# Performance work log

Measured on AMD Instinct MI355X. Metric: run time of the kernel, lower is better.

## Reference

```python
import jax, jax.numpy as jnp
import numpy as np

N = 100000
E = 1600000
F_IN = 64
HID = 64
OUT = 64


def _sage_conv(x, src, dst, w_l, b_l, w_r):
    # PyG SAGEConv (mean aggr): out = lin_l(mean_{j in N(i)} x_j) + lin_r(x_i)
    msgs = x[src]                                             # [E, F] gather
    summed = jax.ops.segment_sum(msgs, dst, num_segments=N)   # [N, F]
    ones = jnp.ones((src.shape[0],), dtype=x.dtype)
    cnt = jax.ops.segment_sum(ones, dst, num_segments=N)      # [N]
    mean = summed / jnp.maximum(cnt, 1.0)[:, None]
    return mean @ w_l + b_l + x @ w_r


def setup_inputs() -> dict:
    key = jax.random.key(0)
    ks = jax.random.split(key, 12)
    sc = lambda f: 1.0 / np.sqrt(f)
    inp = {
        "h": jax.random.normal(ks[0], (N, F_IN), dtype=jnp.float32),
        "edge_index": jax.random.randint(ks[1], (2, E), 0, N, dtype=jnp.int64),
        # conv1: lin_l (with bias) and lin_r (no bias), weights stored [in, out]
        "w1_l": jax.random.normal(ks[2], (F_IN, HID), dtype=jnp.float32) * sc(F_IN),
        "b1_l": jnp.zeros((HID,), dtype=jnp.float32),
        "w1_r": jax.random.normal(ks[3], (F_IN, HID), dtype=jnp.float32) * sc(F_IN),
        "w_lin1": jax.random.normal(ks[4], (HID, HID), dtype=jnp.float32) * sc(HID),
        "b_lin1": jnp.zeros((HID,), dtype=jnp.float32),
        "w2_l": jax.random.normal(ks[5], (HID, HID), dtype=jnp.float32) * sc(HID),
        "b2_l": jnp.zeros((HID,), dtype=jnp.float32),
        "w2_r": jax.random.normal(ks[6], (HID, HID), dtype=jnp.float32) * sc(HID),
        "w_lin2": jax.random.normal(ks[7], (HID, OUT), dtype=jnp.float32) * sc(HID),
        "b_lin2": jnp.zeros((OUT,), dtype=jnp.float32),
    }
    return inp


def reference(h, edge_index, w1_l, b1_l, w1_r, w_lin1, b_lin1,
              w2_l, b2_l, w2_r, w_lin2, b_lin2):
    src, dst = edge_index[0], edge_index[1]
    x = jax.nn.relu(_sage_conv(h, src, dst, w1_l, b1_l, w1_r))
    x = jax.nn.relu(x @ w_lin1 + b_lin1)
    x = jax.nn.relu(_sage_conv(x, src, dst, w2_l, b2_l, w2_r))
    x = x @ w_lin2 + b_lin2
    return x
```

## Files before the change

### kernel.cpp

```cpp
#include <hip/hip_runtime.h>
#include <hip/hip_fp16.h>

#define FEAT   64
#define BSHIFT 8
#define BNODES 256
#define MAXB   512
#define CHUNK  4096
#define REGION 5120
#define ECAP   2048

typedef _Float16 half8 __attribute__((ext_vector_type(8)));
typedef float  float4v __attribute__((ext_vector_type(4)));

__global__ __launch_bounds__(256) void setup_kernel(
    const float* __restrict__ h, __half* __restrict__ h16, int n4, int CB,
    const float* w0, const float* w1, const float* w2,
    const float* w3, const float* w4, const float* w5,
    __half* __restrict__ wT, int* __restrict__ bcur)
{
    int b = blockIdx.x;
    if (b < CB) {
        int i = b * 256 + threadIdx.x;
        if (i < n4) {
            float4 v = ((const float4*)h)[i];
            union { uint2 u; __half2 h2[2]; } r;
            r.h2[0] = __floats2half2_rn(v.x, v.y);
            r.h2[1] = __floats2half2_rn(v.z, v.w);
            ((uint2*)h16)[i] = r.u;
        }
    } else if (b < CB + 96) {
        int bb = b - CB;
        int m = bb >> 4;
        int idx = ((bb & 15) << 8) | threadIdx.x;
        const float* src = m==0?w0 : m==1?w1 : m==2?w2 : m==3?w3 : m==4?w4 : w5;
        int o = idx >> 6, i = idx & 63;
        wT[m * 4096 + o * 64 + i] = __float2half(src[i * 64 + o]);
    } else {
        bcur[threadIdx.x] = 0;
        bcur[threadIdx.x + 256] = 0;
    }
}

__global__ __launch_bounds__(512) void partition_kernel(
    const int* __restrict__ src, const int* __restrict__ dst,
    int* __restrict__ bcur, int* __restrict__ pedge, int E)
{
    __shared__ int cnt[MAXB];
    __shared__ int sa[MAXB], sb[MAXB];
    __shared__ int gb[MAXB];
    __shared__ int lcur[MAXB];
    __shared__ int stage[CHUNK];
    __shared__ int tgt[CHUNK];

    int tid = threadIdx.x;
    cnt[tid] = 0;
    __syncthreads();

    int base = blockIdx.x * CHUNK;
    int vals[8];
    int bs[8];
#pragma unroll
    for (int i = 0; i < 8; i++) {
        int e = base + tid + i * 512;
        bs[i] = -1;
        if (e < E) {
            int s_ = src[e];
            int d_ = dst[e];
            int b  = d_ >> BSHIFT;
            bs[i]  = b;
            vals[i] = s_ | ((d_ & (BNODES - 1)) << 20);
            atomicAdd(&cnt[b], 1);
        }
    }
    __syncthreads();

    sa[tid] = cnt[tid];
    __syncthreads();
    int* cur = sa; int* nxt = sb;
    for (int off = 1; off < MAXB; off <<= 1) {
        nxt[tid] = cur[tid] + ((tid >= off) ? cur[tid - off] : 0);
        __syncthreads();
        int* tmp = cur; cur = nxt; nxt = tmp;
    }
    {
        int c = cnt[tid];
        int lo = cur[tid] - c;
        int gbase = c ? atomicAdd(&bcur[tid], c) : 0;
        if (gbase > REGION) gbase = REGION;
        gb[tid]   = tid * REGION + gbase - lo;
        lcur[tid] = lo;
    }
    __syncthreads();

#pragma unroll
    for (int i = 0; i < 8; i++) {
        if (bs[i] >= 0) {
            int pos = atomicAdd(&lcur[bs[i]], 1);
            stage[pos] = vals[i];
            tgt[pos]   = gb[bs[i]];
        }
    }
    __syncthreads();

    int cn = min(CHUNK, E - base);
    for (int i = tid; i < cn; i += 512)
        pedge[tgt[i] + i] = stage[i];
}

__global__ __launch_bounds__(512) void buildcsr_kernel(
    const int* __restrict__ pedge, const int* __restrict__ bcur,
    unsigned* __restrict__ rowinfo, int* __restrict__ csr, int N)
{
    __shared__ int stg[REGION];
    __shared__ int srt[REGION];
    __shared__ int hist[BNODES], scn[BNODES], lcur[BNODES];
    int b = blockIdx.x;
    int tid = threadIdx.x;
    int beg = b * REGION;
    int cnt = min(bcur[b], REGION);

    if (tid < BNODES) hist[tid] = 0;
    __syncthreads();

    for (int i = tid; i < cnt; i += 512) {
        int p = pedge[beg + i];
        stg[i] = p;
        atomicAdd(&hist[p >> 20], 1);
    }
    __syncthreads();

    int v = 0;
    if (tid < BNODES) { v = hist[tid]; scn[tid] = v; }
    __syncthreads();
    for (int off = 1; off < BNODES; off <<= 1) {
        int t = 0;
        if (tid < BNODES && tid >= off) t = scn[tid - off];
        __syncthreads();
        if (tid < BNODES) scn[tid] += t;
        __syncthreads();
    }
    if (tid < BNODES) {
        int excl = scn[tid] - v;
        int node = (b << BSHIFT) + tid;
        if (node < N)
            rowinfo[node] = (unsigned)(beg + excl) | ((unsigned)v << 21);
        lcur[tid] = excl;
    }
    __syncthreads();

    for (int i = tid; i < cnt; i += 512) {
        int p = stg[i];
        int pos = atomicAdd(&lcur[p >> 20], 1);
        srt[pos] = p & 0xFFFFF;
    }
    __syncthreads();
    for (int i = tid; i < cnt; i += 512)
        csr[beg + i] = srt[i];
}

__global__ __launch_bounds__(256, 4) void fused_layer_kernel(
    const __half* __restrict__ x, const unsigned* __restrict__ rowinfo,
    const int* __restrict__ csr_src,
    const __half* __restrict__ wlT, const __half* __restrict__ wrT,
    const __half* __restrict__ w2T,
    const float* __restrict__ b1, const float* __restrict__ b2,
    float* __restrict__ out_f, __half* __restrict__ out_h,
    int n, int relu_out)
{
    __shared__ __attribute__((aligned(16))) _Float16 sbuf[64][72];
    __shared__ int sedge[ECAP];

    int tid  = threadIdx.x;
    int wave = tid >> 6;
    int lane = tid & 63;
    int sg   = tid >> 4;
    int gg   = (tid >> 3) & 1;
    int s8   = tid & 7;
    int r    = lane & 15;
    int q    = lane >> 4;
    int base = blockIdx.x * 64 + wave * 16;
    int node0 = blockIdx.x * 64;

    int arow = min(base + r, n - 1);
    const half8* xrow = (const half8*)(x + (size_t)arow * FEAT);
    half8 Ax0 = xrow[q], Ax1 = xrow[4 + q];

    unsigned i0 = rowinfo[node0];
    unsigned iL = rowinfo[min(node0 + 63, n - 1)];
    int beg0 = (int)(i0 & 0x1FFFFFu);
    int span = (int)(iL & 0x1FFFFFu) + (int)(iL >> 21) - beg0;

    unsigned infos[4];
#pragma unroll
    for (int i = 0; i < 4; i++) {
        int node = node0 + sg * 4 + i;
        infos[i] = (node < n) ? rowinfo[node] : 0u;
    }

    int spanc = min(span, ECAP);
    for (int i = tid; i < spanc; i += 256)
        sedge[i] = csr_src[beg0 + i];
    __syncthreads();

    int lbeg[4], deg4[4];
    int itmax = 0;
#pragma unroll
    for (int i = 0; i < 4; i++) {
        deg4[i] = (int)(infos[i] >> 21);
        lbeg[i] = deg4[i] ? (int)(infos[i] & 0x1FFFFFu) - beg0 : 0;
        itmax = max(itmax, (deg4[i] + 3) >> 2);
    }
    float acc[4][8];
#pragma unroll
    for (int i = 0; i < 4; i++)
#pragma unroll
        for (int t = 0; t < 8; t++) acc[i][t] = 0.f;

    for (int it = 0; it < itmax; ++it) {
        uint4  rr[8];
        float  ww[8];
#pragma unroll
        for (int i = 0; i < 4; i++) {
            int o0 = (it << 2) + gg;
            int o1 = o0 + 2;
            bool v0 = o0 < deg4[i];
            bool v1 = o1 < deg4[i];
            int l0 = lbeg[i] + (v0 ? o0 : 0);
            int l1 = lbeg[i] + (v1 ? o1 : 0);
            int j0 = v0 ? ((l0 < ECAP) ? sedge[l0] : csr_src[beg0 + l0]) : 0;
            int j1 = v1 ? ((l1 < ECAP) ? sedge[l1] : csr_src[beg0 + l1]) : 0;
            rr[2*i]   = ((const uint4*)(x + (size_t)j0 * FEAT))[s8];
            rr[2*i+1] = ((const uint4*)(x + (size_t)j1 * FEAT))[s8];
            ww[2*i]   = v0 ? 1.0f : 0.0f;
            ww[2*i+1] = v1 ? 1.0f : 0.0f;
        }
#pragma unroll
        for (int k = 0; k < 8; k++) {
            union { uint4 u; __half2 h2[4]; } rv; rv.u = rr[k];
            int a = k >> 1;
#pragma unroll
            for (int t = 0; t < 4; t++) {
                float2 f = __half22float2(rv.h2[t]);
                acc[a][2*t]   = fmaf(ww[k], f.x, acc[a][2*t]);
                acc[a][2*t+1] = fmaf(ww[k], f.y, acc[a][2*t+1]);
            }
        }
    }

#pragma unroll
    for (int i = 0; i < 4; i++) {
#pragma unroll
        for (int t = 0; t < 8; t++)
            acc[i][t] += __shfl_xor(acc[i][t], 8, 64);
        if (gg == 0) {
            int deg = deg4[i];
            float inv = deg ? 1.0f / (float)deg : 0.0f;
            union { uint4 u; __half2 h2[4]; } o;
            o.h2[0] = __floats2half2_rn(acc[i][0]*inv, acc[i][1]*inv);
            o.h2[1] = __floats2half2_rn(acc[i][2]*inv, acc[i][3]*inv);
            o.h2[2] = __floats2half2_rn(acc[i][4]*inv, acc[i][5]*inv);
            o.h2[3] = __floats2half2_rn(acc[i][6]*inv, acc[i][7]*inv);
            int ln = sg * 4 + i;
            *(uint4*)&sbuf[ln][s8 * 8] = o.u;
        }
    }
    __syncthreads();

    union { uint4 u4; half8 h; } Am0u, Am1u;
    Am0u.u4 = *(const uint4*)&sbuf[wave * 16 + r][q * 8];
    Am1u.u4 = *(const uint4*)&sbuf[wave * 16 + r][(4 + q) * 8];

    float4v acc1[4];
#pragma unroll
    for (int c = 0; c < 4; c++) {
        float bv = b1[c * 16 + r];
        acc1[c] = (float4v){bv, bv, bv, bv};
        const half8* bl = (const half8*)(wlT + (size_t)(c * 16 + r) * FEAT);
        const half8* br = (const half8*)(wrT + (size_t)(c * 16 + r) * FEAT);
        acc1[c] = __builtin_amdgcn_mfma_f32_16x16x32_f16(Am0u.h, bl[q],     acc1[c], 0, 0, 0);
        acc1[c] = __builtin_amdgcn_mfma_f32_16x16x32_f16(Am1u.h, bl[4 + q], acc1[c], 0, 0, 0);
        acc1[c] = __builtin_amdgcn_mfma_f32_16x16x32_f16(Ax0,    br[q],     acc1[c], 0, 0, 0);
        acc1[c] = __builtin_amdgcn_mfma_f32_16x16x32_f16(Ax1,    br[4 + q], acc1[c], 0, 0, 0);
    }
#pragma unroll
    for (int c = 0; c < 4; c++)
#pragma unroll
        for (int t = 0; t < 4; t++)
            sbuf[wave * 16 + q * 4 + t][c * 16 + r] = (_Float16)fmaxf(acc1[c][t], 0.0f);
    __syncthreads();

    union { uint4 u4; half8 h; } A2[2];
#pragma unroll
    for (int s = 0; s < 2; s++)
        A2[s].u4 = *(const uint4*)&sbuf[wave * 16 + r][s * 32 + q * 8];

    float4v acc2[4];
#pragma unroll
    for (int c = 0; c < 4; c++) {
        float bv = b2[c * 16 + r];
        acc2[c] = (float4v){bv, bv, bv, bv};
        const half8* bw = (const half8*)(w2T + (size_t)(c * 16 + r) * FEAT);
        acc2[c] = __builtin_amdgcn_mfma_f32_16x16x32_f16(A2[0].h, bw[q],     acc2[c], 0, 0, 0);
        acc2[c] = __builtin_amdgcn_mfma_f32_16x16x32_f16(A2[1].h, bw[4 + q], acc2[c], 0, 0, 0);
    }

#pragma unroll
    for (int c = 0; c < 4; c++)
#pragma unroll
        for (int t = 0; t < 4; t++) {
            int gr = base + q * 4 + t;
            if (gr < n) {
                float v = acc2[c][t];
                if (relu_out) v = fmaxf(v, 0.0f);
                if (out_h) out_h[(size_t)gr * FEAT + c * 16 + r] = __float2half(v);
                else       out_f[(size_t)gr * FEAT + c * 16 + r] = v;
            }
        }
}

extern "C" void kernel_launch(void* const* d_in, const int* in_sizes, int n_in,
                              void* d_out, int out_size, void* d_ws, size_t ws_size,
                              hipStream_t stream) {
    const float* h      = (const float*)d_in[0];
    const int*   ei     = (const int*)d_in[1];
    const float* w1_l   = (const float*)d_in[2];
    const float* b1_l   = (const float*)d_in[3];
    const float* w1_r   = (const float*)d_in[4];
    const float* w_lin1 = (const float*)d_in[5];
    const float* b_lin1 = (const float*)d_in[6];
    const float* w2_l   = (const float*)d_in[7];
    const float* b2_l   = (const float*)d_in[8];
    const float* w2_r   = (const float*)d_in[9];
    const float* w_lin2 = (const float*)d_in[10];
    const float* b_lin2 = (const float*)d_in[11];

    const int N = in_sizes[0] / FEAT;
    const int E = in_sizes[1] / 2;
    const int* src  = ei;
    const int* dst_ = ei + E;

    const int NB = (N + BNODES - 1) >> BSHIFT;
    const int PB = (E + CHUNK - 1) / CHUNK;
    const int n4 = N * FEAT / 4;
    const int CB = (n4 + 255) / 256;
    const int fblk = (N + 63) / 64;

    size_t off = 0;
    int* bcur       = (int*)d_ws + off; off += MAXB;
    unsigned* rowinfo = (unsigned*)((int*)d_ws + off); off += (size_t)N;
    off = (off + 3) & ~(size_t)3;
    int* csr    = (int*)d_ws + off; off += (size_t)NB * REGION + 64;
    off = (off + 3) & ~(size_t)3;
    __half* h16 = (__half*)((int*)d_ws + off); off += (size_t)N * FEAT / 2;
    __half* x2h = (__half*)((int*)d_ws + off); off += (size_t)N * FEAT / 2;
    __half* wT  = (__half*)((int*)d_ws + off); off += 6 * 2048;
    int* pedge  = (int*)d_ws + off; off += (size_t)NB * REGION;

    setup_kernel<<<CB + 96 + 1, 256, 0, stream>>>(
        h, h16, n4, CB, w1_l, w1_r, w_lin1, w2_l, w2_r, w_lin2, wT, bcur);
    partition_kernel<<<PB, 512, 0, stream>>>(src, dst_, bcur, pedge, E);
    buildcsr_kernel<<<NB, 512, 0, stream>>>(pedge, bcur, rowinfo, csr, N);

    fused_layer_kernel<<<fblk, 256, 0, stream>>>(
        h16, rowinfo, csr,
        wT + 0 * 4096, wT + 1 * 4096, wT + 2 * 4096,
        b1_l, b_lin1, (float*)nullptr, x2h, N, 1);

    fused_layer_kernel<<<fblk, 256, 0, stream>>>(
        x2h, rowinfo, csr,
        wT + 3 * 4096, wT + 4 * 4096, wT + 5 * 4096,
        b2_l, b_lin2, (float*)d_out, (__half*)nullptr, N, 0);
}
```

Measured before the change: 237.7 us.

## Merge setup into partition kernel and software-pipeline gathers with zero-row padding

Folds the fp16 conversion and weight transpose into the partition kernel's launch, so those blocks run alongside edge partitioning, and zeroes bcur with a memset instead. In the aggregation loop, the shared-memory CSR staging is dropped and the feature-row gathers are double-buffered: the next iteration's loads and CSR indices are issued before the current ones are consumed. Out-of-range edges now point at an appended zero row, so the masked FMA becomes a plain add. This aims to hide gather latency and save a launch, at the cost of more registers (possible occupancy loss) and uncached CSR index reads.

```diff
diff --git a/kernel.cpp b/kernel.cpp
--- a/kernel.cpp
+++ b/kernel.cpp
@@ -7,43 +7,18 @@
 #define MAXB   512
 #define CHUNK  4096
 #define REGION 5120
-#define ECAP   2048
 
 typedef _Float16 half8 __attribute__((ext_vector_type(8)));
 typedef float  float4v __attribute__((ext_vector_type(4)));
 
-__global__ __launch_bounds__(256) void setup_kernel(
-    const float* __restrict__ h, __half* __restrict__ h16, int n4, int CB,
+__global__ __launch_bounds__(512) void prep_kernel(
+    const int* __restrict__ esrc, const int* __restrict__ edst,
+    int* __restrict__ bcur, int* __restrict__ pedge, int E, int PB,
+    const float* __restrict__ h, __half* __restrict__ h16, __half* __restrict__ x2h,
+    int n4, int CVB, int N,
     const float* w0, const float* w1, const float* w2,
     const float* w3, const float* w4, const float* w5,
-    __half* __restrict__ wT, int* __restrict__ bcur)
-{
-    int b = blockIdx.x;
-    if (b < CB) {
-        int i = b * 256 + threadIdx.x;
-        if (i < n4) {
-            float4 v = ((const float4*)h)[i];
-            union { uint2 u; __half2 h2[2]; } r;
-            r.h2[0] = __floats2half2_rn(v.x, v.y);
-            r.h2[1] = __floats2half2_rn(v.z, v.w);
-            ((uint2*)h16)[i] = r.u;
-        }
-    } else if (b < CB + 96) {
-        int bb = b - CB;
-        int m = bb >> 4;
-        int idx = ((bb & 15) << 8) | threadIdx.x;
-        const float* src = m==0?w0 : m==1?w1 : m==2?w2 : m==3?w3 : m==4?w4 : w5;
-        int o = idx >> 6, i = idx & 63;
-        wT[m * 4096 + o * 64 + i] = __float2half(src[i * 64 + o]);
-    } else {
-        bcur[threadIdx.x] = 0;
-        bcur[threadIdx.x + 256] = 0;
-    }
-}
-
-__global__ __launch_bounds__(512) void partition_kernel(
-    const int* __restrict__ src, const int* __restrict__ dst,
-    int* __restrict__ bcur, int* __restrict__ pedge, int E)
+    __half* __restrict__ wT)
 {
     __shared__ int cnt[MAXB];
     __shared__ int sa[MAXB], sb[MAXB];
@@ -52,11 +27,38 @@
     __shared__ int stage[CHUNK];
     __shared__ int tgt[CHUNK];
 
+    int b   = blockIdx.x;
     int tid = threadIdx.x;
+
+    if (b >= PB) {
+        int bb = b - PB;
+        if (bb < CVB) {
+            int i = bb * 512 + tid;
+            if (i < n4) {
+                float4 v = ((const float4*)h)[i];
+                union { uint2 u; __half2 h2[2]; } r;
+                r.h2[0] = __floats2half2_rn(v.x, v.y);
+                r.h2[1] = __floats2half2_rn(v.z, v.w);
+                ((uint2*)h16)[i] = r.u;
+            }
+        } else if (bb < CVB + 48) {
+            int idx = (bb - CVB) * 512 + tid;
+            int m = idx >> 12;
+            int e = idx & 4095;
+            const float* src = m==0?w0 : m==1?w1 : m==2?w2 : m==3?w3 : m==4?w4 : w5;
+            int o = e >> 6, i = e & 63;
+            wT[m * 4096 + o * 64 + i] = __float2half(src[i * 64 + o]);
+        } else {
+            if (tid < 64)       h16[(size_t)N * FEAT + tid] = __float2half(0.0f);
+            else if (tid < 128) x2h[(size_t)N * FEAT + (tid - 64)] = __float2half(0.0f);
+        }
+        return;
+    }
+
     cnt[tid] = 0;
     __syncthreads();
 
-    int base = blockIdx.x * CHUNK;
+    int base = b * CHUNK;
     int vals[8];
     int bs[8];
 #pragma unroll
@@ -64,12 +66,12 @@
         int e = base + tid + i * 512;
         bs[i] = -1;
         if (e < E) {
-            int s_ = src[e];
-            int d_ = dst[e];
-            int b  = d_ >> BSHIFT;
-            bs[i]  = b;
+            int s_ = esrc[e];
+            int d_ = edst[e];
+            int bk = d_ >> BSHIFT;
+            bs[i]  = bk;
             vals[i] = s_ | ((d_ & (BNODES - 1)) << 20);
-            atomicAdd(&cnt[b], 1);
+            atomicAdd(&cnt[bk], 1);
         }
     }
     __syncthreads();
@@ -168,7 +170,6 @@
     int n, int relu_out)
 {
     __shared__ __attribute__((aligned(16))) _Float16 sbuf[64][72];
-    __shared__ int sedge[ECAP];
 
     int tid  = threadIdx.x;
     int wave = tid >> 6;
@@ -179,36 +180,25 @@
     int r    = lane & 15;
     int q    = lane >> 4;
     int base = blockIdx.x * 64 + wave * 16;
-    int node0 = blockIdx.x * 64;
 
     int arow = min(base + r, n - 1);
     const half8* xrow = (const half8*)(x + (size_t)arow * FEAT);
     half8 Ax0 = xrow[q], Ax1 = xrow[4 + q];
 
-    unsigned i0 = rowinfo[node0];
-    unsigned iL = rowinfo[min(node0 + 63, n - 1)];
-    int beg0 = (int)(i0 & 0x1FFFFFu);
-    int span = (int)(iL & 0x1FFFFFu) + (int)(iL >> 21) - beg0;
-
     unsigned infos[4];
 #pragma unroll
     for (int i = 0; i < 4; i++) {
-        int node = node0 + sg * 4 + i;
+        int node = blockIdx.x * 64 + sg * 4 + i;
         infos[i] = (node < n) ? rowinfo[node] : 0u;
     }
 
-    int spanc = min(span, ECAP);
-    for (int i = tid; i < spanc; i += 256)
-        sedge[i] = csr_src[beg0 + i];
-    __syncthreads();
-
-    int lbeg[4], deg4[4];
+    int lb[4], dg[4];
     int itmax = 0;
 #pragma unroll
     for (int i = 0; i < 4; i++) {
-        deg4[i] = (int)(infos[i] >> 21);
-        lbeg[i] = deg4[i] ? (int)(infos[i] & 0x1FFFFFu) - beg0 : 0;
-        itmax = max(itmax, (deg4[i] + 3) >> 2);
+        dg[i] = (int)(infos[i] >> 21);
+        lb[i] = (int)(infos[i] & 0x1FFFFFu);
+        itmax = max(itmax, (dg[i] + 3) >> 2);
     }
     float acc[4][8];
 #pragma unroll
@@ -216,24 +206,29 @@
 #pragma unroll
         for (int t = 0; t < 8; t++) acc[i][t] = 0.f;
 
-    for (int it = 0; it < itmax; ++it) {
-        uint4  rr[8];
-        float  ww[8];
+    const int nz = n;
+    int ka[4], kb[4];
+    uint4 ra[8], rb[8];
+
+    auto csrf = [&](int itn) {
 #pragma unroll
         for (int i = 0; i < 4; i++) {
-            int o0 = (it << 2) + gg;
-            int o1 = o0 + 2;
-            bool v0 = o0 < deg4[i];
-            bool v1 = o1 < deg4[i];
-            int l0 = lbeg[i] + (v0 ? o0 : 0);
-            int l1 = lbeg[i] + (v1 ? o1 : 0);
-            int j0 = v0 ? ((l0 < ECAP) ? sedge[l0] : csr_src[beg0 + l0]) : 0;
-            int j1 = v1 ? ((l1 < ECAP) ? sedge[l1] : csr_src[beg0 + l1]) : 0;
-            rr[2*i]   = ((const uint4*)(x + (size_t)j0 * FEAT))[s8];
-            rr[2*i+1] = ((const uint4*)(x + (size_t)j1 * FEAT))[s8];
-            ww[2*i]   = v0 ? 1.0f : 0.0f;
-            ww[2*i+1] = v1 ? 1.0f : 0.0f;
-        }
+            int o0 = itn * 4 + gg, o1 = o0 + 2;
+            bool v0 = o0 < dg[i], v1 = o1 < dg[i];
+            int t0 = csr_src[lb[i] + (v0 ? o0 : 0)];
+            int t1 = csr_src[lb[i] + (v1 ? o1 : 0)];
+            ka[i] = v0 ? t0 : nz;
+            kb[i] = v1 ? t1 : nz;
+        }
+    };
+    auto issue = [&](uint4 (&rr)[8]) {
+#pragma unroll
+        for (int i = 0; i < 4; i++) {
+            rr[2*i]   = ((const uint4*)(x + (size_t)ka[i] * FEAT))[s8];
+            rr[2*i+1] = ((const uint4*)(x + (size_t)kb[i] * FEAT))[s8];
+        }
+    };
+    auto consume = [&](uint4 (&rr)[8]) {
 #pragma unroll
         for (int k = 0; k < 8; k++) {
             union { uint4 u; __half2 h2[4]; } rv; rv.u = rr[k];
@@ -241,10 +236,27 @@
 #pragma unroll
             for (int t = 0; t < 4; t++) {
                 float2 f = __half22float2(rv.h2[t]);
-                acc[a][2*t]   = fmaf(ww[k], f.x, acc[a][2*t]);
-                acc[a][2*t+1] = fmaf(ww[k], f.y, acc[a][2*t+1]);
+                acc[a][2*t]   += f.x;
+                acc[a][2*t+1] += f.y;
             }
         }
+    };
+
+    csrf(0);
+    issue(ra);
+    csrf(1);
+
+    int it = 0;
+    while (it < itmax) {
+        issue(rb);
+        csrf(it + 2);
+        consume(ra);
+        ++it;
+        if (it >= itmax) break;
+        issue(ra);
+        csrf(it + 2);
+        consume(rb);
+        ++it;
     }
 
 #pragma unroll
@@ -253,7 +265,7 @@
         for (int t = 0; t < 8; t++)
             acc[i][t] += __shfl_xor(acc[i][t], 8, 64);
         if (gg == 0) {
-            int deg = deg4[i];
+            int deg = dg[i];
             float inv = deg ? 1.0f / (float)deg : 0.0f;
             union { uint4 u; __half2 h2[4]; } o;
             o.h2[0] = __floats2half2_rn(acc[i][0]*inv, acc[i][1]*inv);
@@ -339,10 +351,10 @@
     const int* src  = ei;
     const int* dst_ = ei + E;
 
-    const int NB = (N + BNODES - 1) >> BSHIFT;
-    const int PB = (E + CHUNK - 1) / CHUNK;
-    const int n4 = N * FEAT / 4;
-    const int CB = (n4 + 255) / 256;
+    const int NB  = (N + BNODES - 1) >> BSHIFT;
+    const int PB  = (E + CHUNK - 1) / CHUNK;
+    const int n4  = N * FEAT / 4;
+    const int CVB = (n4 + 511) / 512;
     const int fblk = (N + 63) / 64;
 
     size_t off = 0;
@@ -351,14 +363,16 @@
     off = (off + 3) & ~(size_t)3;
     int* csr    = (int*)d_ws + off; off += (size_t)NB * REGION + 64;
     off = (off + 3) & ~(size_t)3;
-    __half* h16 = (__half*)((int*)d_ws + off); off += (size_t)N * FEAT / 2;
-    __half* x2h = (__half*)((int*)d_ws + off); off += (size_t)N * FEAT / 2;
+    __half* h16 = (__half*)((int*)d_ws + off); off += (size_t)(N + 1) * FEAT / 2;
+    __half* x2h = (__half*)((int*)d_ws + off); off += (size_t)(N + 1) * FEAT / 2;
     __half* wT  = (__half*)((int*)d_ws + off); off += 6 * 2048;
     int* pedge  = (int*)d_ws + off; off += (size_t)NB * REGION;
 
-    setup_kernel<<<CB + 96 + 1, 256, 0, stream>>>(
-        h, h16, n4, CB, w1_l, w1_r, w_lin1, w2_l, w2_r, w_lin2, wT, bcur);
-    partition_kernel<<<PB, 512, 0, stream>>>(src, dst_, bcur, pedge, E);
+    hipMemsetAsync(bcur, 0, MAXB * sizeof(int), stream);
+    prep_kernel<<<PB + CVB + 48 + 1, 512, 0, stream>>>(
+        src, dst_, bcur, pedge, E, PB,
+        h, h16, x2h, n4, CVB, N,
+        w1_l, w1_r, w_lin1, w2_l, w2_r, w_lin2, wT);
     buildcsr_kernel<<<NB, 512, 0, stream>>>(pedge, bcur, rowinfo, csr, N);
 
     fused_layer_kernel<<<fblk, 256, 0, stream>>>(
```

Measured after the change: 274.4 us. 1.15x slower.
